# Performance work log

Hardware: AMD Instinct MI355X
Metric: run time of the kernel (lower is better)

Reference implementation:

```python
import jax, jax.numpy as jnp
import numpy as np

B, T, C, H, N, FFN = 4, 1024, 2048, 32, 64, 7168
HEAD_DIVISOR = 8.0
EPS = 1e-5


def setup_inputs() -> dict:
    key = jax.random.key(0)
    ks = jax.random.split(key, 30)
    rn = lambda k, s, sc=0.02: jax.random.normal(k, s, jnp.float32) * sc
    ru = lambda k, s: jax.random.uniform(k, s, jnp.float32)
    return {
        "x": jax.random.normal(ks[0], (B, T, C), jnp.float32),
        "att_shift": jax.random.normal(ks[1], (B, C), jnp.float32),
        "wkv_state": jax.random.normal(ks[2], (B, H, N, N), jnp.float32) * 0.1,
        "ffn_shift": jax.random.normal(ks[3], (B, C), jnp.float32),
        "ln1_w": jnp.ones((C,), jnp.float32), "ln1_b": jnp.zeros((C,), jnp.float32),
        "ln2_w": jnp.ones((C,), jnp.float32), "ln2_b": jnp.zeros((C,), jnp.float32),
        "mix_k": ru(ks[4], (C,)), "mix_v": ru(ks[5], (C,)),
        "mix_r": ru(ks[6], (C,)), "mix_g": ru(ks[7], (C,)),
        "Wr": rn(ks[8], (C, C)), "Wk": rn(ks[9], (C, C)), "Wv": rn(ks[10], (C, C)),
        "Wg": rn(ks[11], (C, C)), "Wo": rn(ks[12], (C, C)),
        "time_decay": jax.random.normal(ks[13], (H, N), jnp.float32) * 0.5,
        "time_faaaa": jax.random.normal(ks[14], (H, N), jnp.float32) * 0.1,
        "gn_w": jnp.ones((C,), jnp.float32), "gn_b": jnp.zeros((C,), jnp.float32),
        "cmix_k": ru(ks[15], (C,)), "cmix_r": ru(ks[16], (C,)),
        "Wck": rn(ks[17], (C, FFN)), "Wcr": rn(ks[18], (C, C)), "Wcv": rn(ks[19], (FFN, C)),
    }


def _ln(z, w, b):
    m = z.mean(-1, keepdims=True)
    v = z.var(-1, keepdims=True)
    return (z - m) / jnp.sqrt(v + EPS) * w + b


def _shift(x, shift_state):
    # prepend carried last-token state, drop final position
    return jnp.concatenate([shift_state[:, None, :], x[:, :-1]], axis=1)


def reference(x, att_shift, wkv_state, ffn_shift, ln1_w, ln1_b, ln2_w, ln2_b,
              mix_k, mix_v, mix_r, mix_g, Wr, Wk, Wv, Wg, Wo,
              time_decay, time_faaaa, gn_w, gn_b, cmix_k, cmix_r, Wck, Wcr, Wcv):
    Bb, Tt, Cc = x.shape

    # ---- TimeMix ----
    x1 = _ln(x, ln1_w, ln1_b)
    xx = _shift(x1, att_shift)
    xk = x1 * mix_k + xx * (1 - mix_k)
    xv = x1 * mix_v + xx * (1 - mix_v)
    xr = x1 * mix_r + xx * (1 - mix_r)
    xg = x1 * mix_g + xx * (1 - mix_g)
    r = (xr @ Wr).reshape(Bb, Tt, H, N)
    k = (xk @ Wk).reshape(Bb, Tt, H, N)
    v = (xv @ Wv).reshape(Bb, Tt, H, N)
    g = jax.nn.silu(xg @ Wg)

    w = jnp.exp(-jnp.exp(time_decay))[None, :, :, None]  # [1,H,N,1] decay on k-index
    u = time_faaaa[None, :, :, None]                      # [1,H,N,1] bonus on current token

    def step(S, rkv):  # S: [B,H,N,N] (k-index i, v-index j)
        rr, kk, vv = rkv
        kv = kk[..., :, None] * vv[..., None, :]          # [B,H,N,N]
        y = jnp.einsum('bhi,bhij->bhj', rr, S + u * kv)
        return S * w + kv, y

    rkv = (jnp.moveaxis(r, 1, 0), jnp.moveaxis(k, 1, 0), jnp.moveaxis(v, 1, 0))
    new_wkv, ys = jax.lax.scan(step, wkv_state, rkv)      # ys: [T,B,H,N]
    att = jnp.moveaxis(ys, 0, 1)                          # [B,T,H,N]

    # GroupNorm(n_head groups) on att / head_size_divisor
    z = att / HEAD_DIVISOR
    m = z.mean(-1, keepdims=True)
    var = z.var(-1, keepdims=True)
    z = (z - m) / jnp.sqrt(var + EPS)
    z = z * gn_w.reshape(H, N) + gn_b.reshape(H, N)
    att_out = (z.reshape(Bb, Tt, Cc) * g) @ Wo

    x = x + att_out

    # ---- ChannelMix ----
    x2 = _ln(x, ln2_w, ln2_b)
    xx2 = _shift(x2, ffn_shift)
    xck = x2 * cmix_k + xx2 * (1 - cmix_k)
    xcr = x2 * cmix_r + xx2 * (1 - cmix_r)
    kk = jnp.square(jax.nn.relu(xck @ Wck))
    kv = kk @ Wcv
    ffn_out = jax.nn.sigmoid(xcr @ Wcr) * kv
    x = x + ffn_out

    return x, x1[:, -1], new_wkv, x2[:, -1]
```

## Files before the change

kernel.cpp:

```cpp
#include <hip/hip_runtime.h>
#include <cstdint>
#include <cstddef>

typedef unsigned short u16;
typedef unsigned int u32;
typedef short bf16x8 __attribute__((ext_vector_type(8)));
typedef unsigned short u16x4 __attribute__((ext_vector_type(4)));
typedef unsigned short u16x8 __attribute__((ext_vector_type(8)));
typedef float f32x4 __attribute__((ext_vector_type(4)));

#define DEV __device__ __forceinline__

constexpr int Bb = 4, Tt = 1024, Cc = 2048, Hh = 32, Nd = 64, FF = 7168;
constexpr int BT = Bb * Tt;
constexpr int NCH = 16;

DEV u16 f2bf(float f) {
  union { float f; unsigned u; } un; un.f = f;
  unsigned r = un.u + 0x7FFFu + ((un.u >> 16) & 1u);
  return (u16)(r >> 16);
}
DEV float bf2f(u16 h) {
  union { unsigned u; float f; } un; un.u = ((unsigned)h) << 16;
  return un.f;
}
DEV void gll16(const u16* gp, u16* lp) {
  __builtin_amdgcn_global_load_lds(
      (const __attribute__((address_space(1))) unsigned int*)gp,
      (__attribute__((address_space(3))) unsigned int*)lp,
      16, 0, 0);
}
DEV int xcd_swz(int f, int nwg) {
  int q = nwg >> 3;
  return (f & 7) * q + (f >> 3);
}

DEV void transp64_body(const float* __restrict__ W, u16* __restrict__ Wt,
                       int Kk, int Nn) {
  const int n0 = blockIdx.x * 64, k0 = blockIdx.y * 64;
  const int tx = threadIdx.x & 15, ty = threadIdx.x >> 4;
  const int kk = k0 + ty * 4, nn = n0 + tx * 4;
  const float* p = W + (size_t)kk * Nn + nn;
  f32x4 r0 = *(const f32x4*)(p);
  f32x4 r1 = *(const f32x4*)(p + (size_t)Nn);
  f32x4 r2 = *(const f32x4*)(p + 2 * (size_t)Nn);
  f32x4 r3 = *(const f32x4*)(p + 3 * (size_t)Nn);
  #pragma unroll
  for (int j = 0; j < 4; j++) {
    u16x4 o;
    o[0] = f2bf(r0[j]); o[1] = f2bf(r1[j]); o[2] = f2bf(r2[j]); o[3] = f2bf(r3[j]);
    *(u16x4*)(Wt + (size_t)(nn + j) * Kk + kk) = o;
  }
}

__global__ void transp64(const float* __restrict__ W, u16* __restrict__ Wt,
                         int Kk, int Nn) {
  transp64_body(W, Wt, Kk, Nn);
}

__global__ void transp64_6cc(const float* __restrict__ W0, const float* __restrict__ W1,
                             const float* __restrict__ W2, const float* __restrict__ W3,
                             const float* __restrict__ W4, const float* __restrict__ W5,
                             u16* __restrict__ T0, u16* __restrict__ T1,
                             u16* __restrict__ T2, u16* __restrict__ T3,
                             u16* __restrict__ T4, u16* __restrict__ T5) {
  const int z = blockIdx.z;
  const float* W = (z == 0) ? W0 : (z == 1) ? W1 : (z == 2) ? W2 :
                   (z == 3) ? W3 : (z == 4) ? W4 : W5;
  u16* T = (z == 0) ? T0 : (z == 1) ? T1 : (z == 2) ? T2 :
           (z == 3) ? T3 : (z == 4) ? T4 : T5;
  transp64_body(W, T, Cc, Cc);
}

DEV void block_ln(const float* __restrict__ src, int tid, float* red,
                  float vals[8], float& mean, float& inv) {
  float s = 0.f, ss = 0.f;
  #pragma unroll
  for (int i = 0; i < 8; i++) {
    float t = src[tid + i * 256];
    vals[i] = t; s += t; ss += t * t;
  }
  #pragma unroll
  for (int m = 1; m < 64; m <<= 1) { s += __shfl_xor(s, m); ss += __shfl_xor(ss, m); }
  int lane = tid & 63, wv = tid >> 6;
  __syncthreads();
  if (lane == 0) { red[wv] = s; red[4 + wv] = ss; }
  __syncthreads();
  s = red[0] + red[1] + red[2] + red[3];
  ss = red[4] + red[5] + red[6] + red[7];
  mean = s * (1.f / Cc);
  float var = ss * (1.f / Cc) - mean * mean;
  inv = rsqrtf(var + 1e-5f);
}

__global__ __launch_bounds__(256)
void ln_mix4(const float* __restrict__ x, const float* __restrict__ shift,
             const float* __restrict__ w, const float* __restrict__ b,
             const float* __restrict__ mk, const float* __restrict__ mv,
             const float* __restrict__ mr, const float* __restrict__ mg,
             u16* __restrict__ xk, u16* __restrict__ xv,
             u16* __restrict__ xr, u16* __restrict__ xg,
             float* __restrict__ last) {
  int row = blockIdx.x;
  int t = row & (Tt - 1), bb = row >> 10;
  int tid = threadIdx.x;
  __shared__ float red[8];
  const float* cur = x + (size_t)row * Cc;
  float cv[8], pv[8], cm, ci, pm = 0.f, pi = 1.f;
  block_ln(cur, tid, red, cv, cm, ci);
  bool t0 = (t == 0);
  const float* prev = t0 ? (shift + (size_t)bb * Cc) : (cur - Cc);
  if (!t0) {
    block_ln(prev, tid, red, pv, pm, pi);
  } else {
    #pragma unroll
    for (int i = 0; i < 8; i++) pv[i] = prev[tid + i * 256];
  }
  size_t o = (size_t)row * Cc;
  bool isLast = (t == Tt - 1);
  #pragma unroll
  for (int i = 0; i < 8; i++) {
    int c = tid + i * 256;
    float xc = (cv[i] - cm) * ci * w[c] + b[c];
    float xp = t0 ? pv[i] : (pv[i] - pm) * pi * w[c] + b[c];
    xk[o + c] = f2bf(xp + mk[c] * (xc - xp));
    xv[o + c] = f2bf(xp + mv[c] * (xc - xp));
    xr[o + c] = f2bf(xp + mr[c] * (xc - xp));
    xg[o + c] = f2bf(xp + mg[c] * (xc - xp));
    if (isLast) last[(size_t)bb * Cc + c] = xc;
  }
}

__global__ __launch_bounds__(256)
void ln_mix2(const float* __restrict__ x, const float* __restrict__ shift,
             const float* __restrict__ w, const float* __restrict__ b,
             const float* __restrict__ ck, const float* __restrict__ cr,
             u16* __restrict__ xck, u16* __restrict__ xcr,
             float* __restrict__ last) {
  int row = blockIdx.x;
  int t = row & (Tt - 1), bb = row >> 10;
  int tid = threadIdx.x;
  __shared__ float red[8];
  const float* cur = x + (size_t)row * Cc;
  float cv[8], pv[8], cm, ci, pm = 0.f, pi = 1.f;
  block_ln(cur, tid, red, cv, cm, ci);
  bool t0 = (t == 0);
  const float* prev = t0 ? (shift + (size_t)bb * Cc) : (cur - Cc);
  if (!t0) {
    block_ln(prev, tid, red, pv, pm, pi);
  } else {
    #pragma unroll
    for (int i = 0; i < 8; i++) pv[i] = prev[tid + i * 256];
  }
  size_t o = (size_t)row * Cc;
  bool isLast = (t == Tt - 1);
  #pragma unroll
  for (int i = 0; i < 8; i++) {
    int c = tid + i * 256;
    float xc = (cv[i] - cm) * ci * w[c] + b[c];
    float xp = t0 ? pv[i] : (pv[i] - pm) * pi * w[c] + b[c];
    xck[o + c] = f2bf(xp + ck[c] * (xc - xp));
    xcr[o + c] = f2bf(xp + cr[c] * (xc - xp));
    if (isLast) last[(size_t)bb * Cc + c] = xc;
  }
}

DEV int swzoff(int row, int off) {
  return (row << 7) +
         (off ^ ((((row >> 1) & 1) << 4) | (((row >> 2) & 1) << 5) | (((row >> 3) & 1) << 6)));
}

DEV void stage_half(const u16* __restrict__ gbase, int ldK, u16* slot, int tid) {
  #pragma unroll
  for (int c2 = 0; c2 < 2; c2++) {
    const int D = c2 * 8192 + tid * 16;
    const int row = D >> 7;
    const int off = (D & 127) ^ ((((row >> 1) & 1) << 4) | (((row >> 2) & 1) << 5) | (((row >> 3) & 1) << 6));
    gll16(gbase + (size_t)row * ldK + (off >> 1), (u16*)((char*)slot + D));
  }
}

template <int EPI, int NB>
DEV void g256_core(const u16* __restrict__ A, const u16* __restrict__ Bt,
                   int N, int K, int ldK,
                   float* __restrict__ Co, u16* __restrict__ Cb,
                   const float* __restrict__ X1, const float* __restrict__ X2,
                   const u16* __restrict__ X2b,
                   u16 (*lds)[8192], int m0, int n0, int act) {
  const int tid = threadIdx.x;
  const int w = tid >> 6, lane = tid & 63;
  const int l15 = lane & 15, l4 = lane >> 4;
  const int wm = (w & 3) * 64;
  const int wn = (w >> 2) * (NB * 64);
  const int ahalf = wm >> 7;
  const int arow0 = wm & 127;
  const int bhalf = (NB == 2) ? (w >> 2) : 0;
  const int nt = K >> 6;

  const u16* Ag = A + (size_t)m0 * ldK;
  const u16* Bg = Bt + (size_t)n0 * ldK;

  f32x4 acc[4][NB * 4] = {};
  bf16x8 a[4][2];

  stage_half(Ag, ldK, lds[0], tid);
  stage_half(Ag + (size_t)128 * ldK, ldK, lds[1], tid);
  stage_half(Bg, ldK, lds[4], tid);
  if constexpr (NB == 2) stage_half(Bg + (size_t)128 * ldK, ldK, lds[5], tid);
  if (nt > 1) {
    stage_half(Ag + 64, ldK, lds[2], tid);
    stage_half(Ag + (size_t)128 * ldK + 64, ldK, lds[3], tid);
    asm volatile("s_waitcnt vmcnt(4)" ::: "memory");
  } else {
    asm volatile("s_waitcnt vmcnt(0)" ::: "memory");
  }
  asm volatile("s_barrier" ::: "memory");

  for (int t = 0; t < nt; t++) {
    const int buf = t & 1;
    const char* Aslot = (const char*)lds[buf * 2 + ahalf];
    const char* Bslot = (const char*)lds[4 + buf * NB + bhalf];

#define G256_PHASE(p)                                                                       \
    {                                                                                       \
      if constexpr ((p) == 0) {                                                             \
        _Pragma("unroll")                                                                   \
        for (int mf = 0; mf < 4; mf++)                                                      \
          _Pragma("unroll")                                                                 \
          for (int kh = 0; kh < 2; kh++)                                                    \
            a[mf][kh] = *(const bf16x8*)(Aslot +                                            \
                swzoff(arow0 + mf * 16 + l15, kh * 64 + l4 * 16));                          \
      }                                                                                     \
      bf16x8 bfr[NB][2];                                                                    \
      _Pragma("unroll")                                                                     \
      for (int d = 0; d < NB; d++) {                                                        \
        const int jg = (p) * NB + d;                                                        \
        _Pragma("unroll")                                                                   \
        for (int kh = 0; kh < 2; kh++)                                                      \
          bfr[d][kh] = *(const bf16x8*)(Bslot +                                             \
              swzoff((NB == 2 ? 0 : wn) + jg * 16 + l15, kh * 64 + l4 * 16));               \
      }                                                                                     \
      if constexpr ((p) == 0) {                                                             \
        if (t + 1 < nt) stage_half(Bg + (size_t)(t + 1) * 64, ldK,                          \
                                   lds[4 + ((t + 1) & 1) * NB], tid);                       \
      } else if constexpr ((p) == 1) {                                                      \
        if constexpr (NB == 2) {                                                            \
          if (t + 1 < nt) stage_half(Bg + (size_t)128 * ldK + (size_t)(t + 1) * 64, ldK,    \
                                     lds[4 + ((t + 1) & 1) * NB + 1], tid);                 \
        }                                                                                   \
      } else if constexpr ((p) == 2) {                                                      \
        if (t + 2 < nt) stage_half(Ag + (size_t)(t + 2) * 64, ldK, lds[buf << 1], tid);     \
      } else {                                                                              \
        if (t + 2 < nt) stage_half(Ag + (size_t)128 * ldK + (size_t)(t + 2) * 64, ldK,      \
                                   lds[(buf << 1) + 1], tid);                               \
      }                                                                                     \
      __builtin_amdgcn_s_setprio(1);                                                       \
      _Pragma("unroll")                                                                     \
      for (int mf = 0; mf < 4; mf++)                                                        \
        _Pragma("unroll")                                                                   \
        for (int d = 0; d < NB; d++)                                                        \
          _Pragma("unroll")                                                                 \
          for (int kh = 0; kh < 2; kh++)                                                    \
            acc[mf][(p) * NB + d] = __builtin_amdgcn_mfma_f32_16x16x32_bf16(                \
                a[mf][kh], bfr[d][kh], acc[mf][(p) * NB + d], 0, 0, 0);                     \
      __builtin_amdgcn_s_setprio(0);                                                       \
      if constexpr ((p) == 3) {                                                             \
        if (t + 2 < nt) asm volatile("s_waitcnt vmcnt(4)" ::: "memory");                    \
        else            asm volatile("s_waitcnt vmcnt(0)" ::: "memory");                    \
      }                                                                                     \
      asm volatile("s_barrier" ::: "memory");                                               \
    }

    G256_PHASE(0)
    G256_PHASE(1)
    G256_PHASE(2)
    G256_PHASE(3)
#undef G256_PHASE
  }

  #pragma unroll
  for (int mf = 0; mf < 4; mf++) {
    #pragma unroll
    for (int reg = 0; reg < 4; reg++) {
      const int gr = m0 + wm + mf * 16 + l4 * 4 + reg;
      const size_t ro = (size_t)gr * N;
      #pragma unroll
      for (int nf = 0; nf < NB * 4; nf++) {
        const int gc = n0 + wn + nf * 16 + l15;
        float val = acc[mf][nf][reg];
        if constexpr (EPI == 0) {
          Co[ro + gc] = val;
        } else if constexpr (EPI == 1) {
          if (act) val = val / (1.f + __expf(-val));
          Cb[ro + gc] = f2bf(val);
        } else if constexpr (EPI == 3) {
          float tr = fmaxf(val, 0.f);
          Cb[ro + gc] = f2bf(tr * tr);
        } else if constexpr (EPI == 4) {
          Co[ro + gc] = X1[ro + gc] + val;
        } else {
          float s = 1.f / (1.f + __expf(-val));
          float kvv = X2[ro + gc] + bf2f(X2b[ro + gc]);
          Co[ro + gc] = fmaf(s, kvv, X1[ro + gc]);
        }
      }
    }
  }
}

template <int EPI>
__global__ __launch_bounds__(512)
void gemm256s(const u16* __restrict__ A, const u16* __restrict__ Bt,
              int N, int K,
              float* __restrict__ Co, u16* __restrict__ Cb,
              const float* __restrict__ X1, int NX) {
  __shared__ __align__(16) u16 lds[8][8192];
  int o = xcd_swz(blockIdx.x, gridDim.x);
  int xb = o % NX, yb = o / NX;
  g256_core<EPI, 2>(A, Bt, N, K, K, Co, Cb, X1, nullptr, nullptr, lds,
                    yb * 256, xb * 256, 0);
}

template <int EPI>
__global__ __launch_bounds__(512)
void gemm128s(const u16* __restrict__ A, const u16* __restrict__ Bt,
              int N, int K,
              float* __restrict__ Co, u16* __restrict__ Cb,
              const float* __restrict__ X1, const float* __restrict__ X2,
              const u16* __restrict__ X2b, int NX) {
  __shared__ __align__(16) u16 lds[6][8192];
  int o = xcd_swz(blockIdx.x, gridDim.x);
  int xb = o % NX, yb = o / NX;
  g256_core<EPI, 1>(A, Bt, N, K, K, Co, Cb, X1, X2, X2b, lds,
                    yb * 256, xb * 128, 0);
}

__global__ __launch_bounds__(512)
void gemm256_proj(const u16* __restrict__ A0, const u16* __restrict__ A1,
                  const u16* __restrict__ A2, const u16* __restrict__ A3,
                  const u16* __restrict__ B0, const u16* __restrict__ B1,
                  const u16* __restrict__ B2, const u16* __restrict__ B3,
                  u16* __restrict__ C0, u16* __restrict__ C1,
                  u16* __restrict__ C2, u16* __restrict__ C3) {
  __shared__ __align__(16) u16 lds[8][8192];
  int o = xcd_swz(blockIdx.x, gridDim.x);
  int xb = o & 7, yb = (o >> 3) & 15, z = o >> 7;
  const u16* A = (z == 0) ? A0 : (z == 1) ? A1 : (z == 2) ? A2 : A3;
  const u16* Bt = (z == 0) ? B0 : (z == 1) ? B1 : (z == 2) ? B2 : B3;
  u16* Cb = (z == 0) ? C0 : (z == 1) ? C1 : (z == 2) ? C2 : C3;
  g256_core<1, 2>(A, Bt, Cc, Cc, Cc, nullptr, Cb, nullptr, nullptr, nullptr, lds,
                  yb * 256, xb * 256, z == 3);
}

__global__ __launch_bounds__(512)
void gemm256_splitk(const u16* __restrict__ A, const u16* __restrict__ Bt,
                    float* __restrict__ kv0, u16* __restrict__ kv1) {
  __shared__ __align__(16) u16 lds[8][8192];
  int o = xcd_swz(blockIdx.x, gridDim.x);
  int xb = o & 7, yb = (o >> 3) & 15, z = o >> 7;
  const int Koff = z * (FF / 2);
  if (z == 0)
    g256_core<0, 2>(A + Koff, Bt + Koff, Cc, FF / 2, FF, kv0, nullptr,
                    nullptr, nullptr, nullptr, lds, yb * 256, xb * 256, 0);
  else
    g256_core<1, 2>(A + Koff, Bt + Koff, Cc, FF / 2, FF, nullptr, kv1,
                    nullptr, nullptr, nullptr, lds, yb * 256, xb * 256, 0);
}

__global__ __launch_bounds__(256)
void wkv_pre(const u16* __restrict__ rg, const u16* __restrict__ kg,
             const u16* __restrict__ vg, const float* __restrict__ td,
             const float* __restrict__ tf,
             float* __restrict__ Yb, float* __restrict__ Db,
             u16* __restrict__ Rtb) {
  __shared__ float Pt[64][68];
  __shared__ float uL[64];
  __shared__ u16 rB[64 * 72];
  __shared__ u16 kB[64 * 72];
  __shared__ u16 Rh[64 * 72];
  __shared__ u16 KhX[96 * 72];
  __shared__ u16 vA[64 * 72];
  __shared__ u16 Vt[64 * 72];

  const int tid = threadIdx.x, bid = blockIdx.x;
  const int bh = bid >> 4, c = bid & 15;
  const int b = bh >> 5, h = bh & 31;
  const int lane = tid & 63, w = tid >> 6;

  {
    int i = tid & 63;
    float d = __expf(td[h * 64 + i]);
    float c1 = -1.4426950408889634f * d;
    int e0 = (tid >> 6) * 16;
    #pragma unroll
    for (int e = 0; e < 16; e++) Pt[e0 + e][i] = exp2f(c1 * (float)(e0 + e));
    if (tid < 64) uL[tid] = tf[h * 64 + tid];
  }
  __syncthreads();

  const int row = tid >> 2, col0 = (tid & 3) * 16;
  const int tl = row & 15;
  {
    size_t gro = ((size_t)b * Tt + c * 64 + row) * Cc + h * 64 + col0;
    u16x8 rv0 = *(const u16x8*)(rg + gro);
    u16x8 rv1 = *(const u16x8*)(rg + gro + 8);
    u16x8 kv0 = *(const u16x8*)(kg + gro);
    u16x8 kv1 = *(const u16x8*)(kg + gro + 8);
    u16x8 vv0 = *(const u16x8*)(vg + gro);
    u16x8 vv1 = *(const u16x8*)(vg + gro + 8);
    *(u16x8*)&rB[row * 72 + col0] = rv0; *(u16x8*)&rB[row * 72 + col0 + 8] = rv1;
    *(u16x8*)&kB[row * 72 + col0] = kv0; *(u16x8*)&kB[row * 72 + col0 + 8] = kv1;
    *(u16x8*)&vA[row * 72 + col0] = vv0; *(u16x8*)&vA[row * 72 + col0 + 8] = vv1;
    float rf[16], kf[16];
    #pragma unroll
    for (int e = 0; e < 8; e++) { rf[e] = bf2f(rv0[e]); rf[8 + e] = bf2f(rv1[e]); }
    #pragma unroll
    for (int e = 0; e < 8; e++) { kf[e] = bf2f(kv0[e]); kf[8 + e] = bf2f(kv1[e]); }
    u16x8 o0, o1, t0_, t1_;
    #pragma unroll
    for (int e = 0; e < 8; e++) {
      o0[e] = f2bf(rf[e] * Pt[tl][col0 + e]);
      o1[e] = f2bf(rf[8 + e] * Pt[tl][col0 + 8 + e]);
      t0_[e] = f2bf(rf[e] * Pt[row][col0 + e]);
      t1_[e] = f2bf(rf[8 + e] * Pt[row][col0 + 8 + e]);
    }
    *(u16x8*)&Rh[row * 72 + col0] = o0; *(u16x8*)&Rh[row * 72 + col0 + 8] = o1;
    u16* rtp = Rtb + (size_t)bid * 4096 + row * 64 + col0;
    *(u16x8*)rtp = t0_; *(u16x8*)(rtp + 8) = t1_;
    if (row < 48) {
      u16x8 a0, a1;
      #pragma unroll
      for (int e = 0; e < 8; e++) {
        a0[e] = f2bf(kf[e] * Pt[15 - tl][col0 + e]);
        a1[e] = f2bf(kf[8 + e] * Pt[15 - tl][col0 + 8 + e]);
      }
      *(u16x8*)&KhX[row * 72 + col0] = a0; *(u16x8*)&KhX[row * 72 + col0 + 8] = a1;
    }
    if (row < 32) {
      u16x8 a0, a1;
      #pragma unroll
      for (int e = 0; e < 8; e++) {
        a0[e] = f2bf(kf[e] * Pt[31 - tl][col0 + e]);
        a1[e] = f2bf(kf[8 + e] * Pt[31 - tl][col0 + 8 + e]);
      }
      *(u16x8*)&KhX[(48 + row) * 72 + col0] = a0; *(u16x8*)&KhX[(48 + row) * 72 + col0 + 8] = a1;
    }
    if (row < 16) {
      u16x8 a0, a1;
      #pragma unroll
      for (int e = 0; e < 8; e++) {
        a0[e] = f2bf(kf[e] * Pt[47 - tl][col0 + e]);
        a1[e] = f2bf(kf[8 + e] * Pt[47 - tl][col0 + 8 + e]);
      }
      *(u16x8*)&KhX[(80 + row) * 72 + col0] = a0; *(u16x8*)&KhX[(80 + row) * 72 + col0 + 8] = a1;
    }
  }
  __syncthreads();

  {
    const int jj = tid & 63, s0 = (tid >> 6) * 16;
    #pragma unroll
    for (int ds = 0; ds < 16; ds += 2) {
      u32 pk = ((u32)vA[(s0 + ds + 1) * 72 + jj] << 16) | vA[(s0 + ds) * 72 + jj];
      *(u32*)&Vt[jj * 72 + s0 + ds] = pk;
    }
  }
  __syncthreads();

  u16* aB = vA;
  {
    const int pr[6] = {1, 2, 3, 2, 3, 3};
    const int qr[6] = {0, 1, 2, 0, 1, 0};
    const int dr[6] = {0, 0, 0, 1, 1, 2};
    const int lr = lane & 15, kq = lane >> 4;
    for (int pi = w; pi < 6; pi += 4) {
      const int p = pr[pi], q = qr[pi], d = dr[pi];
      const int kbase = (d == 0) ? q * 16 : (d == 1) ? 48 + q * 16 : 80 + q * 16;
      f32x4 aacc = {};
      #pragma unroll
      for (int kf2 = 0; kf2 < 2; kf2++) {
        bf16x8 af = *(const bf16x8*)&Rh[(p * 16 + lr) * 72 + kf2 * 32 + kq * 8];
        bf16x8 bf_ = *(const bf16x8*)&KhX[(kbase + lr) * 72 + kf2 * 32 + kq * 8];
        aacc = __builtin_amdgcn_mfma_f32_16x16x32_bf16(af, bf_, aacc, 0, 0, 0);
      }
      #pragma unroll
      for (int reg = 0; reg < 4; reg++) {
        aB[(p * 16 + kq * 4 + reg) * 72 + q * 16 + lr] = f2bf(aacc[reg]);
        aB[(q * 16 + kq * 4 + reg) * 72 + p * 16 + lr] = 0;
      }
    }
    for (int e = lane; e < 256; e += 64) {
      const int tl2 = e >> 4, sl = e & 15;
      float a = 0.f;
      if (sl <= tl2) {
        const u16* rp = &rB[(w * 16 + tl2) * 72];
        const u16* kp = &kB[(w * 16 + sl) * 72];
        const float* pp = (sl == tl2) ? uL : &Pt[tl2 - 1 - sl][0];
        #pragma unroll
        for (int i0 = 0; i0 < 64; i0 += 4) {
          u16x4 ra = *(const u16x4*)(rp + i0);
          u16x4 ka = *(const u16x4*)(kp + i0);
          f32x4 pa = *(const f32x4*)(pp + i0);
          #pragma unroll
          for (int di = 0; di < 4; di++)
            a = fmaf(bf2f(ra[di]) * bf2f(ka[di]), pa[di], a);
        }
      }
      aB[(w * 16 + tl2) * 72 + w * 16 + sl] = f2bf(a);
    }
  }
  __syncthreads();

  u16* Ktt = KhX;
  {
    const int ii = tid & 63, s0 = (tid >> 6) * 16;
    #pragma unroll
    for (int ds = 0; ds < 16; ds += 2) {
      float v0 = bf2f(kB[(s0 + ds) * 72 + ii]) * Pt[63 - (s0 + ds)][ii];
      float v1 = bf2f(kB[(s0 + ds + 1) * 72 + ii]) * Pt[63 - (s0 + ds + 1)][ii];
      u32 pk = ((u32)f2bf(v1) << 16) | f2bf(v0);
      *(u32*)&Ktt[ii * 72 + s0 + ds] = pk;
    }
  }
  __syncthreads();

  const int lr = lane & 15, kq = lane >> 4;
  {
    f32x4 yac[4] = {};
    #pragma unroll
    for (int kf2 = 0; kf2 < 2; kf2++) {
      bf16x8 af = *(const bf16x8*)&aB[(w * 16 + lr) * 72 + kf2 * 32 + kq * 8];
      #pragma unroll
      for (int nf = 0; nf < 4; nf++) {
        bf16x8 bf_ = *(const bf16x8*)&Vt[(nf * 16 + lr) * 72 + kf2 * 32 + kq * 8];
        yac[nf] = __builtin_amdgcn_mfma_f32_16x16x32_bf16(af, bf_, yac[nf], 0, 0, 0);
      }
    }
    float* Yp = Yb + (size_t)bid * 4096;
    #pragma unroll
    for (int nf = 0; nf < 4; nf++)
      #pragma unroll
      for (int reg = 0; reg < 4; reg++)
        Yp[(w * 16 + kq * 4 + reg) * 64 + nf * 16 + lr] = yac[nf][reg];

    f32x4 dac[4] = {};
    #pragma unroll
    for (int kf2 = 0; kf2 < 2; kf2++) {
      bf16x8 af = *(const bf16x8*)&Ktt[(w * 16 + lr) * 72 + kf2 * 32 + kq * 8];
      #pragma unroll
      for (int nf = 0; nf < 4; nf++) {
        bf16x8 bf_ = *(const bf16x8*)&Vt[(nf * 16 + lr) * 72 + kf2 * 32 + kq * 8];
        dac[nf] = __builtin_amdgcn_mfma_f32_16x16x32_bf16(af, bf_, dac[nf], 0, 0, 0);
      }
    }
    float* Dp = Db + (size_t)bid * 4096;
    #pragma unroll
    for (int nf = 0; nf < 4; nf++)
      #pragma unroll
      for (int reg = 0; reg < 4; reg++)
        Dp[(w * 16 + kq * 4 + reg) * 64 + nf * 16 + lr] = dac[nf][reg];
  }
}

__global__ __launch_bounds__(256)
void wkv_scan(const float* __restrict__ s0g, const float* __restrict__ td,
              const float* __restrict__ Db, u16* __restrict__ Sbb,
              float* __restrict__ sout) {
  const int bh = blockIdx.x, h = bh & 31;
  const int tid = threadIdx.x;
  const int i = tid >> 2, j0 = (tid & 3) * 16;
  float d = __expf(td[h * 64 + i]);
  float w64 = exp2f(-1.4426950408889634f * d * 64.f);
  f32x4 S[4];
  const float* sp = s0g + ((size_t)bh * 64 + i) * 64 + j0;
  #pragma unroll
  for (int q = 0; q < 4; q++) S[q] = *(const f32x4*)(sp + q * 4);
  for (int c = 0; c < NCH; c++) {
    u16* op = Sbb + ((size_t)(bh * 16 + c)) * 4096 + i * 64 + j0;
    u16x8 o0, o1;
    #pragma unroll
    for (int e = 0; e < 4; e++) { o0[e] = f2bf(S[0][e]); o0[4 + e] = f2bf(S[1][e]);
                                  o1[e] = f2bf(S[2][e]); o1[4 + e] = f2bf(S[3][e]); }
    *(u16x8*)op = o0; *(u16x8*)(op + 8) = o1;
    const float* dp = Db + ((size_t)(bh * 16 + c)) * 4096 + i * 64 + j0;
    #pragma unroll
    for (int q = 0; q < 4; q++) {
      f32x4 dv = *(const f32x4*)(dp + q * 4);
      #pragma unroll
      for (int e = 0; e < 4; e++) S[q][e] = fmaf(w64, S[q][e], dv[e]);
    }
  }
  float* fo = sout + ((size_t)bh * 64 + i) * 64 + j0;
  #pragma unroll
  for (int q = 0; q < 4; q++) *(f32x4*)(fo + q * 4) = S[q];
}

__global__ __launch_bounds__(256)
void wkv_post(const u16* __restrict__ Rtb, const u16* __restrict__ Sbb,
              const float* __restrict__ Yb, const u16* __restrict__ g,
              const float* __restrict__ gnw, const float* __restrict__ gnb,
              u16* __restrict__ xo) {
  __shared__ u16 Rt[64 * 72];
  __shared__ u16 St[64 * 72];
  __shared__ u16 xoL[64 * 72];
  const int tid = threadIdx.x, bid = blockIdx.x;
  const int bh = bid >> 4, c = bid & 15;
  const int b = bh >> 5, h = bh & 31;
  const int lane = tid & 63, w = tid >> 6;
  const int row = tid >> 2, col0 = (tid & 3) * 16;

  {
    const u16* rp = Rtb + (size_t)bid * 4096 + row * 64 + col0;
    u16x8 a0 = *(const u16x8*)rp, a1 = *(const u16x8*)(rp + 8);
    *(u16x8*)&Rt[row * 72 + col0] = a0; *(u16x8*)&Rt[row * 72 + col0 + 8] = a1;
  }
  {
    const u16* sp = Sbb + ((size_t)(bh * 16 + c)) * 4096 + row * 64 + col0;
    u16x8 s0 = *(const u16x8*)sp, s1 = *(const u16x8*)(sp + 8);
    #pragma unroll
    for (int e = 0; e < 8; e++) {
      St[(col0 + e) * 72 + row] = s0[e];
      St[(col0 + 8 + e) * 72 + row] = s1[e];
    }
  }
  const int lr = lane & 15, kq = lane >> 4;
  f32x4 acc[4];
  {
    const float* Yp = Yb + (size_t)bid * 4096;
    #pragma unroll
    for (int nf = 0; nf < 4; nf++)
      #pragma unroll
      for (int reg = 0; reg < 4; reg++)
        acc[nf][reg] = Yp[(w * 16 + kq * 4 + reg) * 64 + nf * 16 + lr];
  }
  __syncthreads();
  #pragma unroll
  for (int kf2 = 0; kf2 < 2; kf2++) {
    bf16x8 af = *(const bf16x8*)&Rt[(w * 16 + lr) * 72 + kf2 * 32 + kq * 8];
    #pragma unroll
    for (int nf = 0; nf < 4; nf++) {
      bf16x8 bf_ = *(const bf16x8*)&St[(nf * 16 + lr) * 72 + kf2 * 32 + kq * 8];
      acc[nf] = __builtin_amdgcn_mfma_f32_16x16x32_bf16(af, bf_, acc[nf], 0, 0, 0);
    }
  }
  #pragma unroll
  for (int reg = 0; reg < 4; reg++) {
    float s = 0.f, ss = 0.f;
    #pragma unroll
    for (int nf = 0; nf < 4; nf++) {
      float z = acc[nf][reg] * 0.125f;
      s += z; ss += z * z;
    }
    #pragma unroll
    for (int m = 1; m < 16; m <<= 1) { s += __shfl_xor(s, m); ss += __shfl_xor(ss, m); }
    float mean = s * (1.f / 64.f);
    float var = ss * (1.f / 64.f) - mean * mean;
    float inv = rsqrtf(var + 1e-5f);
    const int tau = w * 16 + kq * 4 + reg;
    #pragma unroll
    for (int nf = 0; nf < 4; nf++) {
      const int col = nf * 16 + lr;
      float z = acc[nf][reg] * 0.125f;
      float zn = (z - mean) * inv * gnw[h * 64 + col] + gnb[h * 64 + col];
      float gv = bf2f(g[((size_t)b * Tt + c * 64 + tau) * Cc + h * 64 + col]);
      xoL[tau * 72 + col] = f2bf(zn * gv);
    }
  }
  __syncthreads();
  {
    u16x8 o0 = *(const u16x8*)&xoL[row * 72 + col0];
    u16x8 o1 = *(const u16x8*)&xoL[row * 72 + col0 + 8];
    u16* xop = xo + ((size_t)b * Tt + c * 64 + row) * Cc + h * 64 + col0;
    *(u16x8*)xop = o0; *(u16x8*)(xop + 8) = o1;
  }
}

extern "C" void kernel_launch(void* const* d_in, const int* in_sizes, int n_in,
                              void* d_out, int out_size, void* d_ws, size_t ws_size,
                              hipStream_t stream) {
  const float* x         = (const float*)d_in[0];
  const float* att_shift = (const float*)d_in[1];
  const float* wkv0      = (const float*)d_in[2];
  const float* ffn_shift = (const float*)d_in[3];
  const float* ln1w = (const float*)d_in[4];
  const float* ln1b = (const float*)d_in[5];
  const float* ln2w = (const float*)d_in[6];
  const float* ln2b = (const float*)d_in[7];
  const float* mixk = (const float*)d_in[8];
  const float* mixv = (const float*)d_in[9];
  const float* mixr = (const float*)d_in[10];
  const float* mixg = (const float*)d_in[11];
  const float* Wr = (const float*)d_in[12];
  const float* Wk = (const float*)d_in[13];
  const float* Wv = (const float*)d_in[14];
  const float* Wg = (const float*)d_in[15];
  const float* Wo = (const float*)d_in[16];
  const float* td = (const float*)d_in[17];
  const float* tf = (const float*)d_in[18];
  const float* gnw = (const float*)d_in[19];
  const float* gnb = (const float*)d_in[20];
  const float* cmk = (const float*)d_in[21];
  const float* cmr = (const float*)d_in[22];
  const float* Wck = (const float*)d_in[23];
  const float* Wcr = (const float*)d_in[24];
  const float* Wcv = (const float*)d_in[25];

  constexpr size_t SZ_CC = (size_t)Cc * Cc * 2;
  constexpr size_t SZ_CF = (size_t)Cc * FF * 2;
  constexpr size_t SZ_AB = (size_t)BT * Cc * 2;
  constexpr size_t O_W   = 0;
  constexpr size_t O_R1  = 6 * SZ_CC + 2 * SZ_CF;
  constexpr size_t R1_SZ = 4 * SZ_AB;
  constexpr size_t O_R2  = O_R1 + R1_SZ;
  constexpr size_t R2_SZ = 3 * SZ_AB;
  constexpr size_t O_R3  = O_R2 + R2_SZ;
  constexpr size_t WS_NEED = O_R3 + SZ_AB;

  if (ws_size < WS_NEED) return;

  char* ws = (char*)d_ws;
  u16* WrT  = (u16*)(ws + O_W);
  u16* WkT  = (u16*)(ws + O_W + 1 * SZ_CC);
  u16* WvT  = (u16*)(ws + O_W + 2 * SZ_CC);
  u16* WgT  = (u16*)(ws + O_W + 3 * SZ_CC);
  u16* WoT  = (u16*)(ws + O_W + 4 * SZ_CC);
  u16* WcrT = (u16*)(ws + O_W + 5 * SZ_CC);
  u16* WckT = (u16*)(ws + O_W + 6 * SZ_CC);
  u16* WcvT = (u16*)(ws + O_W + 6 * SZ_CC + SZ_CF);

  u16*   xk  = (u16*)(ws + O_R1);
  u16*   xv  = (u16*)(ws + O_R1 + SZ_AB);
  u16*   xr  = (u16*)(ws + O_R1 + 2 * SZ_AB);
  u16*   xg  = (u16*)(ws + O_R1 + 3 * SZ_AB);
  float* Yb  = (float*)(ws + O_R1);
  u16*   Rtb = (u16*)(ws + O_R1 + 2 * SZ_AB);
  u16*   Sbb = (u16*)(ws + O_R1 + 3 * SZ_AB);
  u16*   kk  = (u16*)(ws + O_R1);
  u16*   rb  = (u16*)(ws + O_R2);
  u16*   kb  = (u16*)(ws + O_R2 + SZ_AB);
  u16*   vb  = (u16*)(ws + O_R2 + 2 * SZ_AB);
  u16*   xcr = (u16*)(ws + O_R2);
  u16*   xck = (u16*)(ws + O_R2 + SZ_AB);
  u16*   xo  = (u16*)(ws + O_R2 + 2 * SZ_AB);
  float* kv0 = (float*)(ws + O_R2 + SZ_AB);
  u16*   gbuf = (u16*)(ws + O_R3);
  u16*   kv1  = (u16*)(ws + O_R3);

  float* out      = (float*)d_out;
  float* x1_last  = out + (size_t)BT * Cc;
  float* wkv_out  = x1_last + (size_t)Bb * Cc;
  float* x2_last  = wkv_out + (size_t)Bb * Hh * Nd * Nd;
  float* Db       = out;

  transp64_6cc<<<dim3(32, 32, 6), 256, 0, stream>>>(Wr, Wk, Wv, Wg, Wo, Wcr,
                                                    WrT, WkT, WvT, WgT, WoT, WcrT);
  transp64<<<dim3(112, 32), 256, 0, stream>>>(Wck, WckT, Cc, FF);
  transp64<<<dim3(32, 112), 256, 0, stream>>>(Wcv, WcvT, FF, Cc);

  ln_mix4<<<BT, 256, 0, stream>>>(x, att_shift, ln1w, ln1b,
                                  mixk, mixv, mixr, mixg, xk, xv, xr, xg, x1_last);
  gemm256_proj<<<512, 512, 0, stream>>>(xr, xk, xv, xg,
                                        WrT, WkT, WvT, WgT,
                                        rb, kb, vb, gbuf);
  wkv_pre<<<Bb * Hh * NCH, 256, 0, stream>>>(rb, kb, vb, td, tf, Yb, Db, Rtb);
  wkv_scan<<<Bb * Hh, 256, 0, stream>>>(wkv0, td, Db, Sbb, wkv_out);
  wkv_post<<<Bb * Hh * NCH, 256, 0, stream>>>(Rtb, Sbb, Yb, gbuf, gnw, gnb, xo);
  gemm128s<4><<<256, 512, 0, stream>>>(xo, WoT, Cc, Cc, out, nullptr, x,
                                       nullptr, nullptr, 16);
  ln_mix2<<<BT, 256, 0, stream>>>(out, ffn_shift, ln2w, ln2b, cmk, cmr, xck, xcr, x2_last);
  gemm256s<3><<<448, 512, 0, stream>>>(xck, WckT, FF, Cc, nullptr, kk, nullptr, 28);
  gemm256_splitk<<<256, 512, 0, stream>>>(kk, WcvT, kv0, kv1);
  gemm128s<6><<<256, 512, 0, stream>>>(xcr, WcrT, Cc, Cc, out, nullptr, out,
                                       kv0, kv1, 16);

  (void)in_sizes; (void)n_in; (void)out_size;
}
```

Measured before the change: 720.4 us.

## Replace 256x256 K64 GEMM pipeline with 256x128 K32 tiles at higher occupancy

Every GEMM in the block now uses one simpler core with a 256x128 output tile and a K step of 32, double-buffered in a smaller LDS footprint. Launch bounds request four blocks per CU, and grids are doubled to cover the narrower tiles. The intent is to hide latency through occupancy rather than the old four-phase, depth-two prefetch schedule with more register reuse. In exchange, per-tile arithmetic intensity drops, there are twice as many barriers per K, and the full vmcnt(0) wait each iteration may expose load latency.

```diff
diff --git a/kernel.cpp b/kernel.cpp
--- a/kernel.cpp
+++ b/kernel.cpp
@@ -165,117 +165,73 @@
   }
 }
 
-DEV int swzoff(int row, int off) {
-  return (row << 7) +
-         (off ^ ((((row >> 1) & 1) << 4) | (((row >> 2) & 1) << 5) | (((row >> 3) & 1) << 6)));
-}
-
-DEV void stage_half(const u16* __restrict__ gbase, int ldK, u16* slot, int tid) {
-  #pragma unroll
-  for (int c2 = 0; c2 < 2; c2++) {
-    const int D = c2 * 8192 + tid * 16;
-    const int row = D >> 7;
-    const int off = (D & 127) ^ ((((row >> 1) & 1) << 4) | (((row >> 2) & 1) << 5) | (((row >> 3) & 1) << 6));
-    gll16(gbase + (size_t)row * ldK + (off >> 1), (u16*)((char*)slot + D));
-  }
-}
-
-template <int EPI, int NB>
-DEV void g256_core(const u16* __restrict__ A, const u16* __restrict__ Bt,
+DEV int swz32(int row, int off) {
+  return (row << 6) + (off ^ ((((row >> 1) & 1) << 4) | (((row >> 2) & 1) << 5)));
+}
+
+DEV void stageA32(const u16* __restrict__ g, int ldK, u16* slot, int tid) {
+  #pragma unroll
+  for (int p = 0; p < 2; p++) {
+    const int D = p * 8192 + tid * 16;
+    const int row = D >> 6;
+    const int off = (D & 63) ^ ((((row >> 1) & 1) << 4) | (((row >> 2) & 1) << 5));
+    gll16(g + (size_t)row * ldK + (off >> 1), (u16*)((char*)slot + D));
+  }
+}
+DEV void stageB32(const u16* __restrict__ g, int ldK, u16* slot, int tid) {
+  const int D = tid * 16;
+  const int row = D >> 6;
+  const int off = (D & 63) ^ ((((row >> 1) & 1) << 4) | (((row >> 2) & 1) << 5));
+  gll16(g + (size_t)row * ldK + (off >> 1), (u16*)((char*)slot + D));
+}
+
+template <int EPI>
+DEV void gemm_core(const u16* __restrict__ A, const u16* __restrict__ Bt,
                    int N, int K, int ldK,
                    float* __restrict__ Co, u16* __restrict__ Cb,
                    const float* __restrict__ X1, const float* __restrict__ X2,
                    const u16* __restrict__ X2b,
-                   u16 (*lds)[8192], int m0, int n0, int act) {
+                   u16 (*lA)[8192], u16 (*lB)[4096],
+                   int m0, int n0, int act) {
   const int tid = threadIdx.x;
   const int w = tid >> 6, lane = tid & 63;
   const int l15 = lane & 15, l4 = lane >> 4;
-  const int wm = (w & 3) * 64;
-  const int wn = (w >> 2) * (NB * 64);
-  const int ahalf = wm >> 7;
-  const int arow0 = wm & 127;
-  const int bhalf = (NB == 2) ? (w >> 2) : 0;
-  const int nt = K >> 6;
+  const int wm = (w & 3) * 64, wn = (w >> 2) * 64;
+  const int nt = K >> 5;
 
   const u16* Ag = A + (size_t)m0 * ldK;
   const u16* Bg = Bt + (size_t)n0 * ldK;
 
-  f32x4 acc[4][NB * 4] = {};
-  bf16x8 a[4][2];
-
-  stage_half(Ag, ldK, lds[0], tid);
-  stage_half(Ag + (size_t)128 * ldK, ldK, lds[1], tid);
-  stage_half(Bg, ldK, lds[4], tid);
-  if constexpr (NB == 2) stage_half(Bg + (size_t)128 * ldK, ldK, lds[5], tid);
-  if (nt > 1) {
-    stage_half(Ag + 64, ldK, lds[2], tid);
-    stage_half(Ag + (size_t)128 * ldK + 64, ldK, lds[3], tid);
-    asm volatile("s_waitcnt vmcnt(4)" ::: "memory");
-  } else {
-    asm volatile("s_waitcnt vmcnt(0)" ::: "memory");
-  }
+  f32x4 acc[4][4] = {};
+
+  stageA32(Ag, ldK, lA[0], tid);
+  stageB32(Bg, ldK, lB[0], tid);
+  asm volatile("s_waitcnt vmcnt(0)" ::: "memory");
   asm volatile("s_barrier" ::: "memory");
 
   for (int t = 0; t < nt; t++) {
-    const int buf = t & 1;
-    const char* Aslot = (const char*)lds[buf * 2 + ahalf];
-    const char* Bslot = (const char*)lds[4 + buf * NB + bhalf];
-
-#define G256_PHASE(p)                                                                       \
-    {                                                                                       \
-      if constexpr ((p) == 0) {                                                             \
-        _Pragma("unroll")                                                                   \
-        for (int mf = 0; mf < 4; mf++)                                                      \
-          _Pragma("unroll")                                                                 \
-          for (int kh = 0; kh < 2; kh++)                                                    \
-            a[mf][kh] = *(const bf16x8*)(Aslot +                                            \
-                swzoff(arow0 + mf * 16 + l15, kh * 64 + l4 * 16));                          \
-      }                                                                                     \
-      bf16x8 bfr[NB][2];                                                                    \
-      _Pragma("unroll")                                                                     \
-      for (int d = 0; d < NB; d++) {                                                        \
-        const int jg = (p) * NB + d;                                                        \
-        _Pragma("unroll")                                                                   \
-        for (int kh = 0; kh < 2; kh++)                                                      \
-          bfr[d][kh] = *(const bf16x8*)(Bslot +                                             \
-              swzoff((NB == 2 ? 0 : wn) + jg * 16 + l15, kh * 64 + l4 * 16));               \
-      }                                                                                     \
-      if constexpr ((p) == 0) {                                                             \
-        if (t + 1 < nt) stage_half(Bg + (size_t)(t + 1) * 64, ldK,                          \
-                                   lds[4 + ((t + 1) & 1) * NB], tid);                       \
-      } else if constexpr ((p) == 1) {                                                      \
-        if constexpr (NB == 2) {                                                            \
-          if (t + 1 < nt) stage_half(Bg + (size_t)128 * ldK + (size_t)(t + 1) * 64, ldK,    \
-                                     lds[4 + ((t + 1) & 1) * NB + 1], tid);                 \
-        }                                                                                   \
-      } else if constexpr ((p) == 2) {                                                      \
-        if (t + 2 < nt) stage_half(Ag + (size_t)(t + 2) * 64, ldK, lds[buf << 1], tid);     \
-      } else {                                                                              \
-        if (t + 2 < nt) stage_half(Ag + (size_t)128 * ldK + (size_t)(t + 2) * 64, ldK,      \
-                                   lds[(buf << 1) + 1], tid);                               \
-      }                                                                                     \
-      __builtin_amdgcn_s_setprio(1);                                                       \
-      _Pragma("unroll")                                                                     \
-      for (int mf = 0; mf < 4; mf++)                                                        \
-        _Pragma("unroll")                                                                   \
-        for (int d = 0; d < NB; d++)                                                        \
-          _Pragma("unroll")                                                                 \
-          for (int kh = 0; kh < 2; kh++)                                                    \
-            acc[mf][(p) * NB + d] = __builtin_amdgcn_mfma_f32_16x16x32_bf16(                \
-                a[mf][kh], bfr[d][kh], acc[mf][(p) * NB + d], 0, 0, 0);                     \
-      __builtin_amdgcn_s_setprio(0);                                                       \
-      if constexpr ((p) == 3) {                                                             \
-        if (t + 2 < nt) asm volatile("s_waitcnt vmcnt(4)" ::: "memory");                    \
-        else            asm volatile("s_waitcnt vmcnt(0)" ::: "memory");                    \
-      }                                                                                     \
-      asm volatile("s_barrier" ::: "memory");                                               \
-    }
-
-    G256_PHASE(0)
-    G256_PHASE(1)
-    G256_PHASE(2)
-    G256_PHASE(3)
-#undef G256_PHASE
+    const int cur = t & 1;
+    if (t + 1 < nt) {
+      stageA32(Ag + (size_t)(t + 1) * 32, ldK, lA[cur ^ 1], tid);
+      stageB32(Bg + (size_t)(t + 1) * 32, ldK, lB[cur ^ 1], tid);
+    }
+    bf16x8 a[4], b[4];
+    #pragma unroll
+    for (int mf = 0; mf < 4; mf++)
+      a[mf] = *(const bf16x8*)((char*)lA[cur] + swz32(wm + mf * 16 + l15, l4 * 16));
+    #pragma unroll
+    for (int nf = 0; nf < 4; nf++)
+      b[nf] = *(const bf16x8*)((char*)lB[cur] + swz32(wn + nf * 16 + l15, l4 * 16));
+    __builtin_amdgcn_s_setprio(1);
+    #pragma unroll
+    for (int mf = 0; mf < 4; mf++)
+      #pragma unroll
+      for (int nf = 0; nf < 4; nf++)
+        acc[mf][nf] = __builtin_amdgcn_mfma_f32_16x16x32_bf16(
+            a[mf], b[nf], acc[mf][nf], 0, 0, 0);
+    __builtin_amdgcn_s_setprio(0);
+    if (t + 1 < nt) asm volatile("s_waitcnt vmcnt(0)" ::: "memory");
+    asm volatile("s_barrier" ::: "memory");
   }
 
   #pragma unroll
@@ -285,7 +241,7 @@
       const int gr = m0 + wm + mf * 16 + l4 * 4 + reg;
       const size_t ro = (size_t)gr * N;
       #pragma unroll
-      for (int nf = 0; nf < NB * 4; nf++) {
+      for (int nf = 0; nf < 4; nf++) {
         const int gc = n0 + wn + nf * 16 + l15;
         float val = acc[mf][nf][reg];
         if constexpr (EPI == 0) {
@@ -309,62 +265,52 @@
 }
 
 template <int EPI>
-__global__ __launch_bounds__(512)
-void gemm256s(const u16* __restrict__ A, const u16* __restrict__ Bt,
-              int N, int K,
-              float* __restrict__ Co, u16* __restrict__ Cb,
-              const float* __restrict__ X1, int NX) {
-  __shared__ __align__(16) u16 lds[8][8192];
+__global__ __launch_bounds__(512, 4)
+void gemmN(const u16* __restrict__ A, const u16* __restrict__ Bt,
+           int N, int K,
+           float* __restrict__ Co, u16* __restrict__ Cb,
+           const float* __restrict__ X1, const float* __restrict__ X2,
+           const u16* __restrict__ X2b, int NX) {
+  __shared__ __align__(16) u16 lA[2][8192];
+  __shared__ __align__(16) u16 lB[2][4096];
   int o = xcd_swz(blockIdx.x, gridDim.x);
   int xb = o % NX, yb = o / NX;
-  g256_core<EPI, 2>(A, Bt, N, K, K, Co, Cb, X1, nullptr, nullptr, lds,
-                    yb * 256, xb * 256, 0);
-}
-
-template <int EPI>
-__global__ __launch_bounds__(512)
-void gemm128s(const u16* __restrict__ A, const u16* __restrict__ Bt,
-              int N, int K,
-              float* __restrict__ Co, u16* __restrict__ Cb,
-              const float* __restrict__ X1, const float* __restrict__ X2,
-              const u16* __restrict__ X2b, int NX) {
-  __shared__ __align__(16) u16 lds[6][8192];
+  gemm_core<EPI>(A, Bt, N, K, K, Co, Cb, X1, X2, X2b, lA, lB,
+                 yb * 256, xb * 128, 0);
+}
+
+__global__ __launch_bounds__(512, 4)
+void gemm_proj(const u16* __restrict__ A0, const u16* __restrict__ A1,
+               const u16* __restrict__ A2, const u16* __restrict__ A3,
+               const u16* __restrict__ B0, const u16* __restrict__ B1,
+               const u16* __restrict__ B2, const u16* __restrict__ B3,
+               u16* __restrict__ C0, u16* __restrict__ C1,
+               u16* __restrict__ C2, u16* __restrict__ C3) {
+  __shared__ __align__(16) u16 lA[2][8192];
+  __shared__ __align__(16) u16 lB[2][4096];
   int o = xcd_swz(blockIdx.x, gridDim.x);
-  int xb = o % NX, yb = o / NX;
-  g256_core<EPI, 1>(A, Bt, N, K, K, Co, Cb, X1, X2, X2b, lds,
-                    yb * 256, xb * 128, 0);
-}
-
-__global__ __launch_bounds__(512)
-void gemm256_proj(const u16* __restrict__ A0, const u16* __restrict__ A1,
-                  const u16* __restrict__ A2, const u16* __restrict__ A3,
-                  const u16* __restrict__ B0, const u16* __restrict__ B1,
-                  const u16* __restrict__ B2, const u16* __restrict__ B3,
-                  u16* __restrict__ C0, u16* __restrict__ C1,
-                  u16* __restrict__ C2, u16* __restrict__ C3) {
-  __shared__ __align__(16) u16 lds[8][8192];
-  int o = xcd_swz(blockIdx.x, gridDim.x);
-  int xb = o & 7, yb = (o >> 3) & 15, z = o >> 7;
+  int xb = o & 15, yb = (o >> 4) & 15, z = o >> 8;
   const u16* A = (z == 0) ? A0 : (z == 1) ? A1 : (z == 2) ? A2 : A3;
   const u16* Bt = (z == 0) ? B0 : (z == 1) ? B1 : (z == 2) ? B2 : B3;
   u16* Cb = (z == 0) ? C0 : (z == 1) ? C1 : (z == 2) ? C2 : C3;
-  g256_core<1, 2>(A, Bt, Cc, Cc, Cc, nullptr, Cb, nullptr, nullptr, nullptr, lds,
-                  yb * 256, xb * 256, z == 3);
-}
-
-__global__ __launch_bounds__(512)
-void gemm256_splitk(const u16* __restrict__ A, const u16* __restrict__ Bt,
-                    float* __restrict__ kv0, u16* __restrict__ kv1) {
-  __shared__ __align__(16) u16 lds[8][8192];
+  gemm_core<1>(A, Bt, Cc, Cc, Cc, nullptr, Cb, nullptr, nullptr, nullptr,
+               lA, lB, yb * 256, xb * 128, z == 3);
+}
+
+__global__ __launch_bounds__(512, 4)
+void gemm_splitk(const u16* __restrict__ A, const u16* __restrict__ Bt,
+                 float* __restrict__ kv0, u16* __restrict__ kv1) {
+  __shared__ __align__(16) u16 lA[2][8192];
+  __shared__ __align__(16) u16 lB[2][4096];
   int o = xcd_swz(blockIdx.x, gridDim.x);
-  int xb = o & 7, yb = (o >> 3) & 15, z = o >> 7;
+  int xb = o & 15, yb = (o >> 4) & 15, z = o >> 8;
   const int Koff = z * (FF / 2);
   if (z == 0)
-    g256_core<0, 2>(A + Koff, Bt + Koff, Cc, FF / 2, FF, kv0, nullptr,
-                    nullptr, nullptr, nullptr, lds, yb * 256, xb * 256, 0);
+    gemm_core<0>(A + Koff, Bt + Koff, Cc, FF / 2, FF, kv0, nullptr,
+                 nullptr, nullptr, nullptr, lA, lB, yb * 256, xb * 128, 0);
   else
-    g256_core<1, 2>(A + Koff, Bt + Koff, Cc, FF / 2, FF, nullptr, kv1,
-                    nullptr, nullptr, nullptr, lds, yb * 256, xb * 256, 0);
+    gemm_core<1>(A + Koff, Bt + Koff, Cc, FF / 2, FF, nullptr, kv1,
+                 nullptr, nullptr, nullptr, lA, lB, yb * 256, xb * 128, 0);
 }
 
 __global__ __launch_bounds__(256)
@@ -759,19 +705,20 @@
 
   ln_mix4<<<BT, 256, 0, stream>>>(x, att_shift, ln1w, ln1b,
                                   mixk, mixv, mixr, mixg, xk, xv, xr, xg, x1_last);
-  gemm256_proj<<<512, 512, 0, stream>>>(xr, xk, xv, xg,
-                                        WrT, WkT, WvT, WgT,
-                                        rb, kb, vb, gbuf);
+  gemm_proj<<<1024, 512, 0, stream>>>(xr, xk, xv, xg,
+                                      WrT, WkT, WvT, WgT,
+                                      rb, kb, vb, gbuf);
   wkv_pre<<<Bb * Hh * NCH, 256, 0, stream>>>(rb, kb, vb, td, tf, Yb, Db, Rtb);
   wkv_scan<<<Bb * Hh, 256, 0, stream>>>(wkv0, td, Db, Sbb, wkv_out);
   wkv_post<<<Bb * Hh * NCH, 256, 0, stream>>>(Rtb, Sbb, Yb, gbuf, gnw, gnb, xo);
-  gemm128s<4><<<256, 512, 0, stream>>>(xo, WoT, Cc, Cc, out, nullptr, x,
-                                       nullptr, nullptr, 16);
+  gemmN<4><<<256, 512, 0, stream>>>(xo, WoT, Cc, Cc, out, nullptr, x,
+                                    nullptr, nullptr, 16);
   ln_mix2<<<BT, 256, 0, stream>>>(out, ffn_shift, ln2w, ln2b, cmk, cmr, xck, xcr, x2_last);
-  gemm256s<3><<<448, 512, 0, stream>>>(xck, WckT, FF, Cc, nullptr, kk, nullptr, 28);
-  gemm256_splitk<<<256, 512, 0, stream>>>(kk, WcvT, kv0, kv1);
-  gemm128s<6><<<256, 512, 0, stream>>>(xcr, WcrT, Cc, Cc, out, nullptr, out,
-                                       kv0, kv1, 16);
+  gemmN<3><<<896, 512, 0, stream>>>(xck, WckT, FF, Cc, nullptr, kk,
+                                    nullptr, nullptr, nullptr, 56);
+  gemm_splitk<<<512, 512, 0, stream>>>(kk, WcvT, kv0, kv1);
+  gemmN<6><<<256, 512, 0, stream>>>(xcr, WcrT, Cc, Cc, out, nullptr, out,
+                                    kv0, kv1, 16);
 
   (void)in_sizes; (void)n_in; (void)out_size;
 }
```

After: 760.6 us. 1.06x slower.
